# Kernel optimization log

Hardware: AMD Instinct MI355X
Metric: run time of the kernel (lower is better)

## Reference

```python
import jax, jax.numpy as jnp
import numpy as np

H1 = 36
H2 = 1


def _lstm(x, W_ih, W_hh, b_ih, b_hh, H):
    # x: [B, T, D]; W_ih: [4H, D]; W_hh: [4H, H]; biases: [4H]
    # PyTorch gate order: i, f, g, o
    B, T, _ = x.shape
    xg = jnp.einsum('btd,gd->btg', x, W_ih) + (b_ih + b_hh)  # [B, T, 4H]

    def step(carry, xg_t):
        h, c = carry
        g = xg_t + h @ W_hh.T  # [B, 4H]
        i, f, gc, o = jnp.split(g, 4, axis=-1)
        c = jax.nn.sigmoid(f) * c + jax.nn.sigmoid(i) * jnp.tanh(gc)
        h = jax.nn.sigmoid(o) * jnp.tanh(c)
        return (h, c), h

    h0 = jnp.zeros((B, H), x.dtype)
    (_, _), hs = jax.lax.scan(step, (h0, h0), jnp.swapaxes(xg, 0, 1))
    return jnp.swapaxes(hs, 0, 1)  # [B, T, H]


def setup_inputs() -> dict:
    key = jax.random.key(0)
    ks = jax.random.split(key, 9)
    B, T = 2048, 2048
    s1 = 1.0 / np.sqrt(H1)
    s2 = 1.0  # 1/sqrt(hidden_size=1)
    return {
        'x': jax.random.normal(ks[0], (B, T, 1), dtype=jnp.float32),
        'W_ih1': jax.random.uniform(ks[1], (4 * H1, 1), jnp.float32, -s1, s1),
        'W_hh1': jax.random.uniform(ks[2], (4 * H1, H1), jnp.float32, -s1, s1),
        'b_ih1': jax.random.uniform(ks[3], (4 * H1,), jnp.float32, -s1, s1),
        'b_hh1': jax.random.uniform(ks[4], (4 * H1,), jnp.float32, -s1, s1),
        'W_ih2': jax.random.uniform(ks[5], (4 * H2, H1), jnp.float32, -s2, s2),
        'W_hh2': jax.random.uniform(ks[6], (4 * H2, H2), jnp.float32, -s2, s2),
        'b_ih2': jax.random.uniform(ks[7], (4 * H2,), jnp.float32, -s2, s2),
        'b_hh2': jax.random.uniform(ks[8], (4 * H2,), jnp.float32, -s2, s2),
    }


def reference(x, W_ih1, W_hh1, b_ih1, b_hh1, W_ih2, W_hh2, b_ih2, b_hh2):
    h1 = _lstm(x, W_ih1, W_hh1, b_ih1, b_hh1, H1)   # [B, T, 36]
    h1 = jax.nn.relu(h1)
    out = _lstm(h1, W_ih2, W_hh2, b_ih2, b_hh2, H2)  # [B, T, 1]
    return out
```

## Files before the change

kernel.cpp:

```cpp
#include <hip/hip_runtime.h>

namespace {

constexpr int T_LEN = 2048;
constexpr int B_TOT = 2048;
constexpr int H1 = 36;
constexpr int NB = 16;
constexpr int BLOCK = 640;
constexpr int RS = 72;

typedef _Float16 f16x8 __attribute__((ext_vector_type(8)));
typedef _Float16 h16x2 __attribute__((ext_vector_type(2)));
typedef float f32x4 __attribute__((ext_vector_type(4)));

__device__ __forceinline__ float fdot2(float wb, float hb, float acc) {
#if __has_builtin(__builtin_amdgcn_fdot2)
  return __builtin_amdgcn_fdot2(__builtin_bit_cast(h16x2, wb),
                                __builtin_bit_cast(h16x2, hb), acc, false);
#else
  float d;
  asm("v_dot2_f32_f16 %0, %1, %2, %3" : "=v"(d) : "v"(wb), "v"(hb), "0"(acc));
  return d;
#endif
}
__device__ __forceinline__ float pack2h(float a, float b) {
  h16x2 t = {(_Float16)a, (_Float16)b};
  return __builtin_bit_cast(float, t);
}
template <int CTRL>
__device__ __forceinline__ float qb(float v) {
  return __builtin_bit_cast(
      float, __builtin_amdgcn_update_dpp(0, __builtin_bit_cast(int, v), CTRL,
                                         0xf, 0xf, true));
}
__device__ __forceinline__ float fexp2(float x) { return __builtin_amdgcn_exp2f(x); }
__device__ __forceinline__ float frcp(float x) { return __builtin_amdgcn_rcpf(x); }
__device__ __forceinline__ float sigm(float x) { return frcp(1.f + fexp2(x * -1.44269504f)); }
__device__ __forceinline__ float tanh_fast(float x) {
  return fmaf(2.f, frcp(1.f + fexp2(x * -2.88539008f)), -1.f);
}

__device__ __forceinline__ void step_sync() {
  asm volatile("s_waitcnt lgkmcnt(0)" ::: "memory");
  __builtin_amdgcn_s_barrier();
  __builtin_amdgcn_sched_barrier(0);
  asm volatile("" ::: "memory");
}

__global__ __launch_bounds__(BLOCK) void lstm2_kernel(
    const float* __restrict__ x, const float* __restrict__ Wih1,
    const float* __restrict__ Whh1, const float* __restrict__ bih1,
    const float* __restrict__ bhh1, const float* __restrict__ Wih2,
    const float* __restrict__ Whh2, const float* __restrict__ bih2,
    const float* __restrict__ bhh2, float* __restrict__ out)
{
  __shared__ __align__(16) _Float16 lds[2][2][NB][RS];

  const int tid = threadIdx.x;
  const int wid = tid >> 6;
  const int lane = tid & 63;
  const int g0 = blockIdx.x * NB;
  const bool isA = wid < 9;

  for (int i = tid; i < 2 * 2 * NB * RS; i += BLOCK)
    ((_Float16*)lds)[i] = (_Float16)0.f;
  __syncthreads();

  const int m = lane & 15;
  const int q = lane >> 4;
  f16x8 A0 = {}, A1 = {};
  float wxc[4] = {0, 0, 0, 0}, bxc[4] = {0, 0, 0, 0};
  float c1 = 0.f;
  const float* xc = nullptr;
  if (isA) {
    const int u0 = wid * 4;
    const int ra = (m & 3) * H1 + (u0 + (m >> 2));
#pragma unroll
    for (int j = 0; j < 8; ++j) {
      A0[j] = (_Float16)Whh1[ra * H1 + q * 8 + j];
      const int k1 = 32 + q * 8 + j;
      A1[j] = (k1 < H1) ? (_Float16)Whh1[ra * H1 + k1] : (_Float16)0.f;
    }
#pragma unroll
    for (int r = 0; r < 4; ++r) {
      const int rc = r * H1 + (u0 + q);
      wxc[r] = Wih1[rc];
      bxc[r] = bih1[rc] + bhh1[rc];
    }
    xc = x + (size_t)(g0 + m) * T_LEN;
  }

  const int lb = lane >> 2, lg = lane & 3;
  float w2[18];
  float whg = 0.f, b2 = 0.f, c2 = 0.f, h2 = 0.f;
  float* outp = nullptr;
#pragma unroll
  for (int k = 0; k < 18; ++k) w2[k] = 0.f;
  if (!isA) {
    const float* wr = Wih2 + lg * H1;
#pragma unroll
    for (int k = 0; k < 18; ++k) w2[k] = pack2h(wr[2 * k], wr[2 * k + 1]);
    whg = Whh2[lg];
    b2 = bih2[lg] + bhh2[lg];
    outp = out + (size_t)(g0 + lb) * T_LEN;
  }

  float4 qx = make_float4(0.f, 0.f, 0.f, 0.f);
  if (isA) qx = *(const float4*)xc;
  float4 ov = make_float4(0.f, 0.f, 0.f, 0.f);

  auto step = [&](int i, float xv, int s) {
    const int ib = (s + 1) & 1;
    const int wb = s & 1;
    if (isA) {
      const f16x8 B0 = *(const f16x8*)&lds[ib][0][m][q * 8];
      const f16x8 B1 = *(const f16x8*)&lds[ib][0][m][32 + q * 8];
      f32x4 cc;
#pragma unroll
      for (int r = 0; r < 4; ++r) cc[r] = fmaf(xv, wxc[r], bxc[r]);
      cc = __builtin_amdgcn_mfma_f32_16x16x32_f16(A0, B0, cc, 0, 0, 0);
      cc = __builtin_amdgcn_mfma_f32_16x16x32_f16(A1, B1, cc, 0, 0, 0);
      const float I = sigm(cc[0]), F = sigm(cc[1]);
      const float G = tanh_fast(cc[2]), O = sigm(cc[3]);
      c1 = fmaf(F, c1, I * G);
      const float h = O * tanh_fast(c1);
      const int ku = (wid << 2) + q;
      lds[wb][0][m][ku] = (_Float16)h;
      lds[wb][1][m][ku] = (_Float16)fmaxf(h, 0.f);
    } else if (i > 0) {
      const char* rp = (const char*)&lds[ib][1][lb][0];
      const float4 r0 = *(const float4*)rp;
      const float4 r1 = *(const float4*)(rp + 16);
      const float4 r2 = *(const float4*)(rp + 32);
      const float4 r3 = *(const float4*)(rp + 48);
      const float2 r4 = *(const float2*)(rp + 64);
      const float f[18] = {r0.x, r0.y, r0.z, r0.w, r1.x, r1.y, r1.z, r1.w,
                           r2.x, r2.y, r2.z, r2.w, r3.x, r3.y, r3.z, r3.w,
                           r4.x, r4.y};
      float aE = 0.f, aO = 0.f;
#pragma unroll
      for (int k = 0; k < 18; k += 2) aE = fdot2(w2[k], f[k], aE);
#pragma unroll
      for (int k = 1; k < 18; k += 2) aO = fdot2(w2[k], f[k], aO);
      const float pre = (aE + aO) + fmaf(h2, whg, b2);
      const float pI = qb<0x00>(pre);
      const float pF = qb<0x55>(pre);
      const float pG = qb<0xAA>(pre);
      const float pO = qb<0xFF>(pre);
      c2 = fmaf(sigm(pF), c2, sigm(pI) * tanh_fast(pG));
      h2 = sigm(pO) * tanh_fast(c2);
      if (s == 1) ov.x = h2;
      else if (s == 2) ov.y = h2;
      else if (s == 3) ov.z = h2;
      else {
        ov.w = h2;
        if (lg == 0) *(float4*)(outp + (i - 4)) = ov;
      }
    }
    step_sync();
  };

  for (int i0 = 0; i0 < T_LEN; i0 += 4) {
    float4 qn = qx;
    if (isA) {
      const int tn = (i0 + 4 < T_LEN) ? (i0 + 4) : (T_LEN - 4);
      qn = *(const float4*)(xc + tn);
    }
    step(i0 + 0, qx.x, 0);
    step(i0 + 1, qx.y, 1);
    step(i0 + 2, qx.z, 2);
    step(i0 + 3, qx.w, 3);
    qx = qn;
  }
  step(T_LEN, qx.x, 0);
}

}

extern "C" void kernel_launch(void* const* d_in, const int* in_sizes, int n_in,
                              void* d_out, int out_size, void* d_ws, size_t ws_size,
                              hipStream_t stream) {
  const float* x    = (const float*)d_in[0];
  const float* Wih1 = (const float*)d_in[1];
  const float* Whh1 = (const float*)d_in[2];
  const float* bih1 = (const float*)d_in[3];
  const float* bhh1 = (const float*)d_in[4];
  const float* Wih2 = (const float*)d_in[5];
  const float* Whh2 = (const float*)d_in[6];
  const float* bih2 = (const float*)d_in[7];
  const float* bhh2 = (const float*)d_in[8];
  float* out = (float*)d_out;

  dim3 grid(B_TOT / NB);
  dim3 block(BLOCK);
  hipLaunchKernelGGL(lstm2_kernel, grid, block, 0, stream,
                     x, Wih1, Whh1, bih1, bhh1, Wih2, Whh2, bih2, bhh2, out);
}
```

Baseline: 875.5 us.

## Shrink block to four waves with three MFMA tiles per layer-1 wave

Reduces the block from 10 waves to 4: each of 3 layer-1 waves now computes 12 hidden units through three independent MFMA tile pairs, and one wave handles layer 2. The separate ReLU copy in shared memory is removed, and layer 2 applies a packed f16 max when it reads h. The intent is cheaper per-step barriers across fewer waves and more MFMA work in flight per wave. In exchange, each layer-1 wave carries a longer serial chain per step and needs more registers.

Result: slower. 996.6 us (+13.8%).

```diff
diff --git a/kernel.cpp b/kernel.cpp
--- a/kernel.cpp
+++ b/kernel.cpp
@@ -6,7 +6,7 @@
 constexpr int B_TOT = 2048;
 constexpr int H1 = 36;
 constexpr int NB = 16;
-constexpr int BLOCK = 640;
+constexpr int BLOCK = 256;
 constexpr int RS = 72;
 
 typedef _Float16 f16x8 __attribute__((ext_vector_type(8)));
@@ -33,6 +33,11 @@
       float, __builtin_amdgcn_update_dpp(0, __builtin_bit_cast(int, v), CTRL,
                                          0xf, 0xf, true));
 }
+__device__ __forceinline__ float pkrelu(float v) {
+  float r;
+  asm("v_pk_max_f16 %0, %1, %2" : "=v"(r) : "v"(v), "v"(0.f));
+  return r;
+}
 __device__ __forceinline__ float fexp2(float x) { return __builtin_amdgcn_exp2f(x); }
 __device__ __forceinline__ float frcp(float x) { return __builtin_amdgcn_rcpf(x); }
 __device__ __forceinline__ float sigm(float x) { return frcp(1.f + fexp2(x * -1.44269504f)); }
@@ -54,38 +59,43 @@
     const float* __restrict__ Whh2, const float* __restrict__ bih2,
     const float* __restrict__ bhh2, float* __restrict__ out)
 {
-  __shared__ __align__(16) _Float16 lds[2][2][NB][RS];
+  __shared__ __align__(16) _Float16 lds[2][NB][RS];
 
   const int tid = threadIdx.x;
   const int wid = tid >> 6;
   const int lane = tid & 63;
   const int g0 = blockIdx.x * NB;
-  const bool isA = wid < 9;
-
-  for (int i = tid; i < 2 * 2 * NB * RS; i += BLOCK)
+  const bool isA = wid < 3;
+
+  for (int i = tid; i < 2 * NB * RS; i += BLOCK)
     ((_Float16*)lds)[i] = (_Float16)0.f;
   __syncthreads();
 
   const int m = lane & 15;
   const int q = lane >> 4;
-  f16x8 A0 = {}, A1 = {};
-  float wxc[4] = {0, 0, 0, 0}, bxc[4] = {0, 0, 0, 0};
-  float c1 = 0.f;
+  f16x8 A0[3] = {}, A1[3] = {};
+  float wxc[3][4] = {}, bxc[3][4] = {};
+  float c1v[3] = {0.f, 0.f, 0.f};
   const float* xc = nullptr;
+  int ku0 = 0;
   if (isA) {
-    const int u0 = wid * 4;
-    const int ra = (m & 3) * H1 + (u0 + (m >> 2));
-#pragma unroll
-    for (int j = 0; j < 8; ++j) {
-      A0[j] = (_Float16)Whh1[ra * H1 + q * 8 + j];
-      const int k1 = 32 + q * 8 + j;
-      A1[j] = (k1 < H1) ? (_Float16)Whh1[ra * H1 + k1] : (_Float16)0.f;
-    }
-#pragma unroll
-    for (int r = 0; r < 4; ++r) {
-      const int rc = r * H1 + (u0 + q);
-      wxc[r] = Wih1[rc];
-      bxc[r] = bih1[rc] + bhh1[rc];
+    ku0 = wid * 12 + q * 3;
+#pragma unroll
+    for (int t = 0; t < 3; ++t) {
+      const int uA = wid * 12 + (m >> 2) * 3 + t;
+      const int ra = (m & 3) * H1 + uA;
+#pragma unroll
+      for (int j = 0; j < 8; ++j) {
+        A0[t][j] = (_Float16)Whh1[ra * H1 + q * 8 + j];
+        const int k1 = 32 + q * 8 + j;
+        A1[t][j] = (k1 < H1) ? (_Float16)Whh1[ra * H1 + k1] : (_Float16)0.f;
+      }
+#pragma unroll
+      for (int r = 0; r < 4; ++r) {
+        const int rc = r * H1 + (wid * 12 + q * 3 + t);
+        wxc[t][r] = Wih1[rc];
+        bxc[t][r] = bih1[rc] + bhh1[rc];
+      }
     }
     xc = x + (size_t)(g0 + m) * T_LEN;
   }
@@ -113,30 +123,40 @@
     const int ib = (s + 1) & 1;
     const int wb = s & 1;
     if (isA) {
-      const f16x8 B0 = *(const f16x8*)&lds[ib][0][m][q * 8];
-      const f16x8 B1 = *(const f16x8*)&lds[ib][0][m][32 + q * 8];
-      f32x4 cc;
-#pragma unroll
-      for (int r = 0; r < 4; ++r) cc[r] = fmaf(xv, wxc[r], bxc[r]);
-      cc = __builtin_amdgcn_mfma_f32_16x16x32_f16(A0, B0, cc, 0, 0, 0);
-      cc = __builtin_amdgcn_mfma_f32_16x16x32_f16(A1, B1, cc, 0, 0, 0);
-      const float I = sigm(cc[0]), F = sigm(cc[1]);
-      const float G = tanh_fast(cc[2]), O = sigm(cc[3]);
-      c1 = fmaf(F, c1, I * G);
-      const float h = O * tanh_fast(c1);
-      const int ku = (wid << 2) + q;
-      lds[wb][0][m][ku] = (_Float16)h;
-      lds[wb][1][m][ku] = (_Float16)fmaxf(h, 0.f);
+      const f16x8 B0 = *(const f16x8*)&lds[ib][m][q * 8];
+      const f16x8 B1 = *(const f16x8*)&lds[ib][m][32 + q * 8];
+      f32x4 cc[3];
+#pragma unroll
+      for (int t = 0; t < 3; ++t)
+#pragma unroll
+        for (int r = 0; r < 4; ++r) cc[t][r] = fmaf(xv, wxc[t][r], bxc[t][r]);
+#pragma unroll
+      for (int t = 0; t < 3; ++t)
+        cc[t] = __builtin_amdgcn_mfma_f32_16x16x32_f16(A0[t], B0, cc[t], 0, 0, 0);
+#pragma unroll
+      for (int t = 0; t < 3; ++t)
+        cc[t] = __builtin_amdgcn_mfma_f32_16x16x32_f16(A1[t], B1, cc[t], 0, 0, 0);
+#pragma unroll
+      for (int t = 0; t < 3; ++t) {
+        const float I = sigm(cc[t][0]), F = sigm(cc[t][1]);
+        const float G = tanh_fast(cc[t][2]), O = sigm(cc[t][3]);
+        c1v[t] = fmaf(F, c1v[t], I * G);
+        const float h = O * tanh_fast(c1v[t]);
+        lds[wb][m][ku0 + t] = (_Float16)h;
+      }
     } else if (i > 0) {
-      const char* rp = (const char*)&lds[ib][1][lb][0];
+      const char* rp = (const char*)&lds[ib][lb][0];
       const float4 r0 = *(const float4*)rp;
       const float4 r1 = *(const float4*)(rp + 16);
       const float4 r2 = *(const float4*)(rp + 32);
       const float4 r3 = *(const float4*)(rp + 48);
       const float2 r4 = *(const float2*)(rp + 64);
-      const float f[18] = {r0.x, r0.y, r0.z, r0.w, r1.x, r1.y, r1.z, r1.w,
-                           r2.x, r2.y, r2.z, r2.w, r3.x, r3.y, r3.z, r3.w,
-                           r4.x, r4.y};
+      const float f[18] = {
+          pkrelu(r0.x), pkrelu(r0.y), pkrelu(r0.z), pkrelu(r0.w),
+          pkrelu(r1.x), pkrelu(r1.y), pkrelu(r1.z), pkrelu(r1.w),
+          pkrelu(r2.x), pkrelu(r2.y), pkrelu(r2.z), pkrelu(r2.w),
+          pkrelu(r3.x), pkrelu(r3.y), pkrelu(r3.z), pkrelu(r3.w),
+          pkrelu(r4.x), pkrelu(r4.y)};
       float aE = 0.f, aO = 0.f;
 #pragma unroll
       for (int k = 0; k < 18; k += 2) aE = fdot2(w2[k], f[k], aE);
```

## Fold input, bias and activation scaling into MFMA weights; restructure gate math

Applied to the files above, without the earlier changes.

Folds the input-weight term and bias into the second MFMA by storing x (split into hi/lo fp16) and constant ones in spare LDS columns of the hidden-state buffer. Pre-scales the weights by -log2(e) (or -2log2(e) for the g gate) so the activations need no multiply, and merges sigmoid/tanh into one lstm_unit that tracks a scaled cell state. Only one wave loads x and writes it to LDS each step. Layer 2 uses four independent dot accumulators for more ILP. The risk is fp16 precision loss on the scaled weights and bias; the hi/lo splits are meant to limit it.

New measurement: 791.9 us. 1.11x faster.

```diff
diff --git a/kernel.cpp b/kernel.cpp
--- a/kernel.cpp
+++ b/kernel.cpp
@@ -35,9 +35,17 @@
 }
 __device__ __forceinline__ float fexp2(float x) { return __builtin_amdgcn_exp2f(x); }
 __device__ __forceinline__ float frcp(float x) { return __builtin_amdgcn_rcpf(x); }
-__device__ __forceinline__ float sigm(float x) { return frcp(1.f + fexp2(x * -1.44269504f)); }
-__device__ __forceinline__ float tanh_fast(float x) {
-  return fmaf(2.f, frcp(1.f + fexp2(x * -2.88539008f)), -1.f);
+
+__device__ __forceinline__ float lstm_unit(float pi, float pf, float pg, float po,
+                                           float& cS) {
+  const float I = frcp(1.f + fexp2(pi));
+  const float F = frcp(1.f + fexp2(pf));
+  const float O = frcp(1.f + fexp2(po));
+  const float rG = frcp(1.f + fexp2(pg));
+  const float Gs = fmaf(rG, -5.77078016f, 2.88539008f);
+  cS = fmaf(F, cS, I * Gs);
+  const float rC = frcp(1.f + fexp2(cS));
+  return fmaf(rC, O + O, -O);
 }
 
 __device__ __forceinline__ void step_sync() {
@@ -59,74 +67,97 @@
   const int tid = threadIdx.x;
   const int wid = tid >> 6;
   const int lane = tid & 63;
+  const int m = lane & 15;
+  const int q = lane >> 4;
   const int g0 = blockIdx.x * NB;
   const bool isA = wid < 9;
 
   for (int i = tid; i < 2 * 2 * NB * RS; i += BLOCK)
     ((_Float16*)lds)[i] = (_Float16)0.f;
   __syncthreads();
-
-  const int m = lane & 15;
-  const int q = lane >> 4;
+  if (tid < NB) {
+    lds[0][0][tid][38] = (_Float16)1.f;
+    lds[0][0][tid][39] = (_Float16)1.f;
+    lds[1][0][tid][38] = (_Float16)1.f;
+    lds[1][0][tid][39] = (_Float16)1.f;
+    const float x0 = x[(size_t)(g0 + tid) * T_LEN];
+    const _Float16 xh0 = (_Float16)x0;
+    lds[1][0][tid][36] = xh0;
+    lds[1][0][tid][37] = (_Float16)(x0 - (float)xh0);
+  }
+  __syncthreads();
+
   f16x8 A0 = {}, A1 = {};
-  float wxc[4] = {0, 0, 0, 0}, bxc[4] = {0, 0, 0, 0};
   float c1 = 0.f;
-  const float* xc = nullptr;
+  int ku = 0;
   if (isA) {
     const int u0 = wid * 4;
+    ku = u0 + q;
+    const float sga = ((m & 3) == 2) ? -2.88539008f : -1.44269504f;
     const int ra = (m & 3) * H1 + (u0 + (m >> 2));
 #pragma unroll
-    for (int j = 0; j < 8; ++j) {
-      A0[j] = (_Float16)Whh1[ra * H1 + q * 8 + j];
-      const int k1 = 32 + q * 8 + j;
-      A1[j] = (k1 < H1) ? (_Float16)Whh1[ra * H1 + k1] : (_Float16)0.f;
+    for (int j = 0; j < 8; ++j)
+      A0[j] = (_Float16)(sga * Whh1[ra * H1 + q * 8 + j]);
+#pragma unroll
+    for (int j = 0; j < 8; ++j) A1[j] = (_Float16)0.f;
+    if (q == 0) {
+#pragma unroll
+      for (int j = 0; j < 4; ++j)
+        A1[j] = (_Float16)(sga * Whh1[ra * H1 + 32 + j]);
+      const _Float16 wih = (_Float16)(sga * Wih1[ra]);
+      A1[4] = wih;
+      A1[5] = wih;
+      const float bb = sga * (bih1[ra] + bhh1[ra]);
+      const _Float16 bh = (_Float16)bb;
+      A1[6] = bh;
+      A1[7] = (_Float16)(bb - (float)bh);
     }
-#pragma unroll
-    for (int r = 0; r < 4; ++r) {
-      const int rc = r * H1 + (u0 + q);
-      wxc[r] = Wih1[rc];
-      bxc[r] = bih1[rc] + bhh1[rc];
-    }
+  }
+
+  const float* xc = nullptr;
+  float4 qx = make_float4(0.f, 0.f, 0.f, 0.f);
+  if (wid == 8) {
     xc = x + (size_t)(g0 + m) * T_LEN;
+    qx = *(const float4*)xc;
   }
 
   const int lb = lane >> 2, lg = lane & 3;
   float w2[18];
-  float whg = 0.f, b2 = 0.f, c2 = 0.f, h2 = 0.f;
+  float whg = 0.f, b2 = 0.f, c2S = 0.f, h2 = 0.f;
   float* outp = nullptr;
 #pragma unroll
   for (int k = 0; k < 18; ++k) w2[k] = 0.f;
-  if (!isA) {
+  if (wid == 9) {
+    const float s2 = (lg == 2) ? -2.88539008f : -1.44269504f;
     const float* wr = Wih2 + lg * H1;
 #pragma unroll
-    for (int k = 0; k < 18; ++k) w2[k] = pack2h(wr[2 * k], wr[2 * k + 1]);
-    whg = Whh2[lg];
-    b2 = bih2[lg] + bhh2[lg];
+    for (int k = 0; k < 18; ++k)
+      w2[k] = pack2h(s2 * wr[2 * k], s2 * wr[2 * k + 1]);
+    whg = s2 * Whh2[lg];
+    b2 = s2 * (bih2[lg] + bhh2[lg]);
     outp = out + (size_t)(g0 + lb) * T_LEN;
   }
 
-  float4 qx = make_float4(0.f, 0.f, 0.f, 0.f);
-  if (isA) qx = *(const float4*)xc;
   float4 ov = make_float4(0.f, 0.f, 0.f, 0.f);
-
-  auto step = [&](int i, float xv, int s) {
+  const f32x4 z4 = {0.f, 0.f, 0.f, 0.f};
+
+  auto step = [&](int i, int s, float xw) {
     const int ib = (s + 1) & 1;
     const int wb = s & 1;
     if (isA) {
       const f16x8 B0 = *(const f16x8*)&lds[ib][0][m][q * 8];
       const f16x8 B1 = *(const f16x8*)&lds[ib][0][m][32 + q * 8];
-      f32x4 cc;
-#pragma unroll
-      for (int r = 0; r < 4; ++r) cc[r] = fmaf(xv, wxc[r], bxc[r]);
-      cc = __builtin_amdgcn_mfma_f32_16x16x32_f16(A0, B0, cc, 0, 0, 0);
+      f32x4 cc = __builtin_amdgcn_mfma_f32_16x16x32_f16(A0, B0, z4, 0, 0, 0);
       cc = __builtin_amdgcn_mfma_f32_16x16x32_f16(A1, B1, cc, 0, 0, 0);
-      const float I = sigm(cc[0]), F = sigm(cc[1]);
-      const float G = tanh_fast(cc[2]), O = sigm(cc[3]);
-      c1 = fmaf(F, c1, I * G);
-      const float h = O * tanh_fast(c1);
-      const int ku = (wid << 2) + q;
-      lds[wb][0][m][ku] = (_Float16)h;
-      lds[wb][1][m][ku] = (_Float16)fmaxf(h, 0.f);
+      const float h = lstm_unit(cc[0], cc[1], cc[2], cc[3], c1);
+      const _Float16 hh = (_Float16)h;
+      lds[wb][0][m][ku] = hh;
+      lds[wb][1][m][ku] = (hh > (_Float16)0.f) ? hh : (_Float16)0.f;
+      if (wid == 8 && q == 0) {
+        const _Float16 xh = (_Float16)xw;
+        h16x2 xp = {xh, (_Float16)(xw - (float)xh)};
+        *(h16x2*)&lds[wb][0][m][36] = xp;
+      }
     } else if (i > 0) {
       const char* rp = (const char*)&lds[ib][1][lb][0];
       const float4 r0 = *(const float4*)rp;
@@ -137,18 +168,25 @@
       const float f[18] = {r0.x, r0.y, r0.z, r0.w, r1.x, r1.y, r1.z, r1.w,
                            r2.x, r2.y, r2.z, r2.w, r3.x, r3.y, r3.z, r3.w,
                            r4.x, r4.y};
-      float aE = 0.f, aO = 0.f;
-#pragma unroll
-      for (int k = 0; k < 18; k += 2) aE = fdot2(w2[k], f[k], aE);
-#pragma unroll
-      for (int k = 1; k < 18; k += 2) aO = fdot2(w2[k], f[k], aO);
-      const float pre = (aE + aO) + fmaf(h2, whg, b2);
+      float a0 = fdot2(w2[0], f[0], fmaf(h2, whg, b2));
+      float a1 = fdot2(w2[1], f[1], 0.f);
+      float a2 = fdot2(w2[2], f[2], 0.f);
+      float a3 = fdot2(w2[3], f[3], 0.f);
+#pragma unroll
+      for (int k = 4; k < 16; k += 4) {
+        a0 = fdot2(w2[k], f[k], a0);
+        a1 = fdot2(w2[k + 1], f[k + 1], a1);
+        a2 = fdot2(w2[k + 2], f[k + 2], a2);
+        a3 = fdot2(w2[k + 3], f[k + 3], a3);
+      }
+      a0 = fdot2(w2[16], f[16], a0);
+      a1 = fdot2(w2[17], f[17], a1);
+      const float pre = (a0 + a2) + (a1 + a3);
       const float pI = qb<0x00>(pre);
       const float pF = qb<0x55>(pre);
       const float pG = qb<0xAA>(pre);
       const float pO = qb<0xFF>(pre);
-      c2 = fmaf(sigm(pF), c2, sigm(pI) * tanh_fast(pG));
-      h2 = sigm(pO) * tanh_fast(c2);
+      h2 = lstm_unit(pI, pF, pG, pO, c2S);
       if (s == 1) ov.x = h2;
       else if (s == 2) ov.y = h2;
       else if (s == 3) ov.z = h2;
@@ -162,17 +200,17 @@
 
   for (int i0 = 0; i0 < T_LEN; i0 += 4) {
     float4 qn = qx;
-    if (isA) {
+    if (wid == 8) {
       const int tn = (i0 + 4 < T_LEN) ? (i0 + 4) : (T_LEN - 4);
       qn = *(const float4*)(xc + tn);
     }
-    step(i0 + 0, qx.x, 0);
-    step(i0 + 1, qx.y, 1);
-    step(i0 + 2, qx.z, 2);
-    step(i0 + 3, qx.w, 3);
+    step(i0 + 0, 0, qx.y);
+    step(i0 + 1, 1, qx.z);
+    step(i0 + 2, 2, qx.w);
+    step(i0 + 3, 3, qn.x);
     qx = qn;
   }
-  step(T_LEN, qx.x, 0);
+  step(T_LEN, 0, qx.y);
 }
 
 }
```
